# Kernel tuning notes

Hardware: AMD Instinct MI355X
Metric: run time of the kernel (lower is better)

Reference implementation:

```python
import jax, jax.numpy as jnp
import numpy as np
import math

B, S, D, H, DFF = 2, 2048, 1024, 16, 4096
DK = D // H
EPS = 1e-5


def setup_inputs() -> dict:
    key = jax.random.key(0)
    ks = jax.random.split(key, 8)
    s = 0.02
    return {
        "x": jax.random.normal(ks[0], (B, S, D), jnp.float32),
        "src_mask": jnp.ones((B, 1, 1, S), jnp.int32),
        "wq": jax.random.normal(ks[1], (D, D), jnp.float32) * s,
        "bq": jnp.zeros((D,), jnp.float32),
        "wk": jax.random.normal(ks[2], (D, D), jnp.float32) * s,
        "bk": jnp.zeros((D,), jnp.float32),
        "wv": jax.random.normal(ks[3], (D, D), jnp.float32) * s,
        "bv": jnp.zeros((D,), jnp.float32),
        "wo": jax.random.normal(ks[4], (D, D), jnp.float32) * s,
        "bo": jnp.zeros((D,), jnp.float32),
        "w1": jax.random.normal(ks[5], (DFF, D), jnp.float32) * s,
        "b1": jnp.zeros((DFF,), jnp.float32),
        "w2": jax.random.normal(ks[6], (D, DFF), jnp.float32) * s,
        "b2": jnp.zeros((D,), jnp.float32),
        "alpha1": jnp.ones((1,), jnp.float32),
        "bias1": jnp.ones((1,), jnp.float32),
        "alpha2": jnp.ones((1,), jnp.float32),
        "bias2": jnp.ones((1,), jnp.float32),
    }


def _layernorm(x, alpha, bias):
    # Faithful to source: unbiased std (ddof=1), divide by (std + eps),
    # scalar alpha/bias both initialized to 1.
    mean = jnp.mean(x, axis=-1, keepdims=True)
    std = jnp.std(x, axis=-1, keepdims=True, ddof=1)
    return alpha * (x - mean) / (std + EPS) + bias


def _mha(x, wq, bq, wk, bk, wv, bv, wo, bo):
    q = (x @ wq.T + bq).reshape(B, S, H, DK).swapaxes(1, 2)  # b h s d
    k = (x @ wk.T + bk).reshape(B, S, H, DK).swapaxes(1, 2)
    v = (x @ wv.T + bv).reshape(B, S, H, DK).swapaxes(1, 2)
    scores = jnp.einsum("bhqd,bhkd->bhqk", q, k) / math.sqrt(DK)
    # NOTE: source calls masked_fill (out-of-place) and discards the result,
    # so the mask has NO effect. Reproduced faithfully: no masking here.
    attn = jax.nn.softmax(scores, axis=-1)
    out = jnp.einsum("bhqk,bhkd->bhqd", attn, v)
    out = out.swapaxes(1, 2).reshape(B, S, D)
    return out @ wo.T + bo


def reference(x, src_mask, wq, bq, wk, bk, wv, bv, wo, bo,
              w1, b1, w2, b2, alpha1, bias1, alpha2, bias2):
    # residual[0]: x + attn(norm(x)) (dropout=0 -> identity)
    h1 = x + _mha(_layernorm(x, alpha1, bias1), wq, bq, wk, bk, wv, bv, wo, bo)
    # residual[1]: h1 + ffn(norm(h1))
    n2 = _layernorm(h1, alpha2, bias2)
    ffn = (n2 @ w1.T + b1) @ w2.T + b2
    return h1 + ffn
```

## Files before the change

kernel.cpp:

```cpp
#include <hip/hip_runtime.h>
#include <stdint.h>

#define Bx   2
#define Sx   2048
#define Dx   1024
#define Hx   16
#define DKx  64
#define DFFx 4096
#define Mx   4096

#define CEXP 0.18033688011112042f

typedef __attribute__((ext_vector_type(8))) short short8;
typedef __attribute__((ext_vector_type(4))) float f32x4;
typedef __attribute__((ext_vector_type(4))) unsigned short ushort4v;

__device__ __forceinline__ unsigned short f2b(float f) {
    union { float f; uint32_t u; } v; v.f = f;
    uint32_t u = v.u;
    u += 0x7fffu + ((u >> 16) & 1u);
    return (unsigned short)(u >> 16);
}

__device__ __forceinline__ float fexp2(float x) {
#if __has_builtin(__builtin_amdgcn_exp2f)
    return __builtin_amdgcn_exp2f(x);
#else
    return exp2f(x);
#endif
}

__global__ __launch_bounds__(256) void conv_all(
    const float4* __restrict__ wq, const float4* __restrict__ wk,
    const float4* __restrict__ wv, const float4* __restrict__ wo,
    const float4* __restrict__ w1, const float4* __restrict__ w2,
    const float4* __restrict__ bq, const float4* __restrict__ bk,
    const float4* __restrict__ bv,
    ushort4v* __restrict__ dqkv, ushort4v* __restrict__ dwo,
    ushort4v* __restrict__ d1, ushort4v* __restrict__ d2,
    float4* __restrict__ dbias) {
    const int i = blockIdx.x * 256 + threadIdx.x;
    const int S4 = 1 << 18;
    if (i < 4 * S4) {
        const float4* s; ushort4v* d;
        if (i < S4)          { s = wq + i;            d = dqkv + i; }
        else if (i < 2 * S4) { s = wk + (i - S4);     d = dqkv + i; }
        else if (i < 3 * S4) { s = wv + (i - 2 * S4); d = dqkv + i; }
        else                 { s = wo + (i - 3 * S4); d = dwo + (i - 3 * S4); }
        const float4 v = *s;
        ushort4v o; o.x = f2b(v.x); o.y = f2b(v.y); o.z = f2b(v.z); o.w = f2b(v.w);
        *d = o;
    } else if (i < 8 * S4) {
        const float4 v = w1[i - 4 * S4];
        ushort4v o; o.x = f2b(v.x); o.y = f2b(v.y); o.z = f2b(v.z); o.w = f2b(v.w);
        d1[i - 4 * S4] = o;
    } else if (i < 12 * S4) {
        const float4 v = w2[i - 8 * S4];
        ushort4v o; o.x = f2b(v.x); o.y = f2b(v.y); o.z = f2b(v.z); o.w = f2b(v.w);
        d2[i - 8 * S4] = o;
    } else if (i < 12 * S4 + 768) {
        const int jn = i - 12 * S4;
        dbias[jn] = (jn < 256) ? bq[jn] : (jn < 512 ? bk[jn - 256] : bv[jn - 512]);
    }
}

__global__ __launch_bounds__(256) void layernorm_k(const float* __restrict__ x,
                                                   const float* __restrict__ alpha,
                                                   const float* __restrict__ beta,
                                                   unsigned short* __restrict__ out) {
    __shared__ float red[8];
    const int row = blockIdx.x;
    const int t = threadIdx.x, lane = t & 63, w = t >> 6;
    float4 v = ((const float4*)(x + (size_t)row * Dx))[t];
    float s = v.x + v.y + v.z + v.w;
    float q = v.x*v.x + v.y*v.y + v.z*v.z + v.w*v.w;
#pragma unroll
    for (int off = 1; off < 64; off <<= 1) {
        s += __shfl_xor(s, off);
        q += __shfl_xor(q, off);
    }
    if (lane == 0) { red[w] = s; red[4 + w] = q; }
    __syncthreads();
    s = red[0] + red[1] + red[2] + red[3];
    q = red[4] + red[5] + red[6] + red[7];
    const float mean = s * (1.0f / Dx);
    float var = (q - (float)Dx * mean * mean) * (1.0f / (Dx - 1));
    var = fmaxf(var, 0.0f);
    const float inv = alpha[0] / (sqrtf(var) + 1e-5f);
    const float bb = beta[0];
    ushort4v o;
    o.x = f2b((v.x - mean) * inv + bb);
    o.y = f2b((v.y - mean) * inv + bb);
    o.z = f2b((v.z - mean) * inv + bb);
    o.w = f2b((v.w - mean) * inv + bb);
    *(ushort4v*)(out + (size_t)row * Dx + t * 4) = o;
}

#define GLDS(gp, lp) __builtin_amdgcn_global_load_lds( \
    (const __attribute__((address_space(1))) unsigned int*)(gp), \
    (__attribute__((address_space(3))) unsigned int*)(lp), 16, 0, 0)

#define STAGE(buf, kt) do {                                                     \
    const int k0_ = (kt) << 5;                                                  \
    _Pragma("unroll")                                                           \
    for (int i_ = 0; i_ < MB/2; ++i_) {                                         \
      const int ca_ = (MB==4) ? (w*2 + i_) : w;                                 \
      GLDS(A + (size_t)(bm + ca_*16 + srow)*K + k0_ + skc*8, &As[buf][ca_*512]);\
    }                                                                           \
    _Pragma("unroll")                                                           \
    for (int i_ = 0; i_ < 2; ++i_) {                                            \
      const int cb_ = w*2 + i_;                                                 \
      GLDS(W + (size_t)(bn + cb_*16 + srow)*K + k0_ + skc*8, &Bs[buf][cb_*512]);\
    }                                                                           \
  } while (0)

template<int BM>
__global__ __launch_bounds__(256) void gemm2(const short* __restrict__ A,
                                             const short* __restrict__ W,
                                             const float* __restrict__ bias,
                                             const float* __restrict__ res,
                                             float* __restrict__ Cout,
                                             int M, int N, int K) {
    constexpr int MB = BM / 32;
    __shared__ alignas(16) short As[2][BM * 32];
    __shared__ alignas(16) short Bs[2][128 * 32];
    const int t = threadIdx.x, lane = t & 63, w = t >> 6;
    const int bb = blockIdx.x, xcd = bb & 7, jj = bb >> 3;
    const int bn = (jj & 7) * 128;
    const int bm = (xcd * 8 + (jj >> 3)) * BM;
    const int wm = (w >> 1) * (BM / 2), wn = (w & 1) * 64;
    const int srow = lane >> 2, skc = lane & 3;

    f32x4 acc[MB][4] = {};
    const int nkt = K >> 5;

    STAGE(0, 0);
    __syncthreads();
    int cur = 0;
    for (int kt = 0; kt < nkt; ++kt) {
        if (kt + 1 < nkt) STAGE(cur ^ 1, kt + 1);
        const short* as = &As[cur][0];
        const short* bs = &Bs[cur][0];
        short8 af[MB], bfr[4];
#pragma unroll
        for (int mb = 0; mb < MB; ++mb)
            af[mb] = *(const short8*)&as[(wm + mb * 16 + (lane & 15)) * 32 + (lane >> 4) * 8];
#pragma unroll
        for (int nb = 0; nb < 4; ++nb)
            bfr[nb] = *(const short8*)&bs[(wn + nb * 16 + (lane & 15)) * 32 + (lane >> 4) * 8];
#pragma unroll
        for (int mb = 0; mb < MB; ++mb)
#pragma unroll
            for (int nb = 0; nb < 4; ++nb)
                acc[mb][nb] = __builtin_amdgcn_mfma_f32_16x16x32_bf16(af[mb], bfr[nb], acc[mb][nb], 0, 0, 0);
        __syncthreads();
        cur ^= 1;
    }

    const int r0 = (lane >> 4) * 4, c0 = lane & 15;
#pragma unroll
    for (int mb = 0; mb < MB; ++mb)
#pragma unroll
        for (int nb = 0; nb < 4; ++nb) {
            const int col = bn + wn + nb * 16 + c0;
            const float bv = bias[col];
            const int row0 = bm + wm + mb * 16 + r0;
#pragma unroll
            for (int r = 0; r < 4; ++r) {
                const size_t idx = (size_t)(row0 + r) * N + col;
                Cout[idx] = acc[mb][nb][r] + bv + res[idx];
            }
        }
}

template<int MODE>
__global__ __launch_bounds__(256) void gemm128(const short* __restrict__ A,
                                               const short* __restrict__ W,
                                               const float* __restrict__ bias,
                                               void* __restrict__ Cout,
                                               int N, int K,
                                               unsigned short* __restrict__ Qout,
                                               unsigned short* __restrict__ Kout,
                                               unsigned short* __restrict__ Vout) {
    constexpr int MB = 4;
    __shared__ alignas(16) short As[2][128 * 32];
    __shared__ alignas(16) short Bs[2][128 * 32];
    const int t = threadIdx.x, lane = t & 63, w = t >> 6;
    const int bb = blockIdx.x, bpx = gridDim.x >> 3;
    const int g = (bb & 7) * bpx + (bb >> 3);
    const int bn = (g >> 5) * 128;
    const int bm = (g & 31) * 128;
    const int wm = (w >> 1) * 64, wn = (w & 1) * 64;
    const int srow = lane >> 2, skc = lane & 3;

    f32x4 acc[MB][4] = {};
    const int nkt = K >> 5;

    STAGE(0, 0);
    __syncthreads();
    int cur = 0;
    for (int kt = 0; kt < nkt; ++kt) {
        if (kt + 1 < nkt) STAGE(cur ^ 1, kt + 1);
        const short* as = &As[cur][0];
        const short* bs = &Bs[cur][0];
        short8 af[MB], bfr[4];
#pragma unroll
        for (int mb = 0; mb < MB; ++mb)
            af[mb] = *(const short8*)&as[(wm + mb * 16 + (lane & 15)) * 32 + (lane >> 4) * 8];
#pragma unroll
        for (int nb = 0; nb < 4; ++nb)
            bfr[nb] = *(const short8*)&bs[(wn + nb * 16 + (lane & 15)) * 32 + (lane >> 4) * 8];
#pragma unroll
        for (int mb = 0; mb < MB; ++mb)
#pragma unroll
            for (int nb = 0; nb < 4; ++nb)
                acc[mb][nb] = __builtin_amdgcn_mfma_f32_16x16x32_bf16(af[mb], bfr[nb], acc[mb][nb], 0, 0, 0);
        __syncthreads();
        cur ^= 1;
    }

    const int r0 = (lane >> 4) * 4, c0 = lane & 15;
#pragma unroll
    for (int mb = 0; mb < MB; ++mb)
#pragma unroll
        for (int nb = 0; nb < 4; ++nb) {
            const int col = bn + wn + nb * 16 + c0;
            const float bv = bias[col];
            const int row0 = bm + wm + mb * 16 + r0;
            if (MODE == 0) {
#pragma unroll
                for (int r = 0; r < 4; ++r)
                    ((unsigned short*)Cout)[(size_t)(row0 + r) * N + col] = f2b(acc[mb][nb][r] + bv);
            } else {
                if (col < 1024) {
#pragma unroll
                    for (int r = 0; r < 4; ++r)
                        Qout[(size_t)(row0 + r) * 1024 + col] = f2b((acc[mb][nb][r] + bv) * CEXP);
                } else if (col < 2048) {
#pragma unroll
                    for (int r = 0; r < 4; ++r)
                        Kout[(size_t)(row0 + r) * 1024 + (col - 1024)] = f2b(acc[mb][nb][r] + bv);
                } else {
                    const int dk = col - 2048, hh = dk >> 6, dlo = dk & 63;
                    const int bbv = row0 >> 11, s0 = row0 & 2047;
                    const int vrow = (bbv * 16 + hh) * 64 + dlo;
                    ushort4v pv;
                    pv.x = f2b(acc[mb][nb][0] + bv);
                    pv.y = f2b(acc[mb][nb][1] + bv);
                    pv.z = f2b(acc[mb][nb][2] + bv);
                    pv.w = f2b(acc[mb][nb][3] + bv);
                    *(ushort4v*)&Vout[(size_t)vrow * Sx + s0] = pv;
                }
            }
        }
}

__global__ __launch_bounds__(256) void gemmsk(const short* __restrict__ A,
                                              const short* __restrict__ W,
                                              float* __restrict__ P0,
                                              float* __restrict__ P1,
                                              int K) {
    constexpr int MB = 4;
    __shared__ alignas(16) short As[2][128 * 32];
    __shared__ alignas(16) short Bs[2][128 * 32];
    const int t = threadIdx.x, lane = t & 63, w = t >> 6;
    const int bb = blockIdx.x, xcd = bb & 7, jj = bb >> 3;
    const int bn = (jj & 7) * 128;
    const int p = (xcd << 3) | (jj >> 3);
    const int bm = (p & 31) * 128;
    const int kz = p >> 5;
    float* __restrict__ P = kz ? P1 : P0;
    const int wm = (w >> 1) * 64, wn = (w & 1) * 64;
    const int srow = lane >> 2, skc = lane & 3;

    f32x4 acc[MB][4] = {};
    const int nkt = (K >> 1) >> 5;
    const int kbeg = kz * nkt;

    STAGE(0, kbeg);
    __syncthreads();
    int cur = 0;
    for (int kt = kbeg; kt < kbeg + nkt; ++kt) {
        if (kt + 1 < kbeg + nkt) STAGE(cur ^ 1, kt + 1);
        const short* as = &As[cur][0];
        const short* bs = &Bs[cur][0];
        short8 af[MB], bfr[4];
#pragma unroll
        for (int mb = 0; mb < MB; ++mb)
            af[mb] = *(const short8*)&as[(wm + mb * 16 + (lane & 15)) * 32 + (lane >> 4) * 8];
#pragma unroll
        for (int nb = 0; nb < 4; ++nb)
            bfr[nb] = *(const short8*)&bs[(wn + nb * 16 + (lane & 15)) * 32 + (lane >> 4) * 8];
#pragma unroll
        for (int mb = 0; mb < MB; ++mb)
#pragma unroll
            for (int nb = 0; nb < 4; ++nb)
                acc[mb][nb] = __builtin_amdgcn_mfma_f32_16x16x32_bf16(af[mb], bfr[nb], acc[mb][nb], 0, 0, 0);
        __syncthreads();
        cur ^= 1;
    }

    const int r0 = (lane >> 4) * 4, c0 = lane & 15;
#pragma unroll
    for (int mb = 0; mb < MB; ++mb)
#pragma unroll
        for (int nb = 0; nb < 4; ++nb) {
            const int col = bn + wn + nb * 16 + c0;
            const int row0 = bm + wm + mb * 16 + r0;
#pragma unroll
            for (int r = 0; r < 4; ++r)
                P[(size_t)(row0 + r) * Dx + col] = acc[mb][nb][r];
        }
}

__global__ __launch_bounds__(256) void epi2(const float4* __restrict__ p0,
                                            const float4* __restrict__ p1,
                                            const float4* __restrict__ b2,
                                            const float4* __restrict__ h1,
                                            float4* __restrict__ out) {
    const int i = blockIdx.x * 256 + threadIdx.x;
    const float4 bv = b2[i & 255];
    const float4 a = p0[i], b = p1[i], h = h1[i];
    float4 o;
    o.x = a.x + b.x + h.x + bv.x;
    o.y = a.y + b.y + h.y + bv.y;
    o.z = a.z + b.z + h.z + bv.z;
    o.w = a.w + b.w + h.w + bv.w;
    out[i] = o;
}

__global__ __launch_bounds__(256) void attn_fwd4(const short* __restrict__ Q,
                                                 const short* __restrict__ Kg,
                                                 const short* __restrict__ Vtg,
                                                 unsigned short* __restrict__ O) {
    __shared__ alignas(16) short Ks[64 * 64];
    __shared__ alignas(16) short Vs[64 * 64];
    __shared__ alignas(16) short Pl[4][32 * 64];
    const int t = threadIdx.x, lane = t & 63, w = t >> 6;
    const int bh = blockIdx.x;
    const int b = bh >> 4, h = bh & 15;
    const int q0 = blockIdx.y * 128 + w * 32;
    const int lo = lane & 15, hi = lane >> 4;

    short8 qf[2][2];
#pragma unroll
    for (int mb = 0; mb < 2; ++mb)
#pragma unroll
        for (int kf = 0; kf < 2; ++kf)
            qf[mb][kf] = *(const short8*)&Q[(size_t)(b * Sx + q0 + mb * 16 + lo) * Dx
                                            + h * DKx + kf * 32 + hi * 8];

    f32x4 o_[2][4] = {};
    f32x4 l_acc[2] = {};
    short8 ones;
#pragma unroll
    for (int j = 0; j < 8; ++j) ones[j] = (short)0x3F80;

    const int srow = t >> 2;
    const int scol2 = (t & 3) * 32;
    const int swz = (srow & 7) << 4;
    const short* Kbase = Kg + (size_t)(b * Sx) * Dx + h * DKx;
    const short* Vbase = Vtg + (size_t)(bh * 64 + srow) * Sx;
    char* KsB = (char*)Ks;
    char* VsB = (char*)Vs;
    char* PwB = (char*)&Pl[w][0];

    short8 kr0, kr1, vr0, vr1;
    {
        const short* kp = Kbase + (size_t)srow * Dx + (t & 3) * 16;
        kr0 = *(const short8*)kp; kr1 = *(const short8*)(kp + 8);
        const short* vp = Vbase + (t & 3) * 16;
        vr0 = *(const short8*)vp; vr1 = *(const short8*)(vp + 8);
    }

    for (int kt = 0; kt < Sx / 64; ++kt) {
        __syncthreads();
        *(short8*)(KsB + ((srow * 128 + scol2) ^ swz)) = kr0;
        *(short8*)(KsB + ((srow * 128 + scol2 + 16) ^ swz)) = kr1;
        *(short8*)(VsB + ((srow * 128 + scol2) ^ swz)) = vr0;
        *(short8*)(VsB + ((srow * 128 + scol2 + 16) ^ swz)) = vr1;
        __syncthreads();
        if (kt + 1 < Sx / 64) {
            const short* kp = Kbase + (size_t)((kt + 1) * 64 + srow) * Dx + (t & 3) * 16;
            kr0 = *(const short8*)kp; kr1 = *(const short8*)(kp + 8);
            const short* vp = Vbase + (kt + 1) * 64 + (t & 3) * 16;
            vr0 = *(const short8*)vp; vr1 = *(const short8*)(vp + 8);
        }

        f32x4 s[2][4] = {};
        __builtin_amdgcn_s_setprio(1);
#pragma unroll
        for (int nb = 0; nb < 4; ++nb) {
            const int key = nb * 16 + lo;
            const int ksw = (key & 7) << 4;
#pragma unroll
            for (int kf = 0; kf < 2; ++kf) {
                const short8 kfr = *(const short8*)(KsB + ((key * 128 + kf * 64 + hi * 16) ^ ksw));
#pragma unroll
                for (int mb = 0; mb < 2; ++mb)
                    s[mb][nb] = __builtin_amdgcn_mfma_f32_16x16x32_bf16(qf[mb][kf], kfr, s[mb][nb], 0, 0, 0);
            }
        }
        __builtin_amdgcn_s_setprio(0);

#pragma unroll
        for (int mb = 0; mb < 2; ++mb)
#pragma unroll
            for (int nb = 0; nb < 4; ++nb) {
                const int k = nb * 16 + lo;
#pragma unroll
                for (int r = 0; r < 4; ++r) {
                    const float p = fexp2(s[mb][nb][r]);
                    union { float f; uint32_t u; } cv; cv.f = p;
                    const int qq = mb * 16 + hi * 4 + r;
                    *(short*)(PwB + ((qq * 128 + k * 2) ^ ((qq & 7) << 4))) = (short)(cv.u >> 16);
                }
            }

        short8 pa[2][2];
#pragma unroll
        for (int mb = 0; mb < 2; ++mb)
#pragma unroll
            for (int kc = 0; kc < 2; ++kc)
                pa[mb][kc] = *(const short8*)(PwB + (((mb * 16 + lo) * 128 + kc * 64 + hi * 16) ^ ((lo & 7) << 4)));

        __builtin_amdgcn_s_setprio(1);
#pragma unroll
        for (int mb = 0; mb < 2; ++mb) {
            l_acc[mb] = __builtin_amdgcn_mfma_f32_16x16x32_bf16(pa[mb][0], ones, l_acc[mb], 0, 0, 0);
            l_acc[mb] = __builtin_amdgcn_mfma_f32_16x16x32_bf16(pa[mb][1], ones, l_acc[mb], 0, 0, 0);
        }

#pragma unroll
        for (int d = 0; d < 4; ++d) {
            const int vd = d * 16 + lo;
            const int vsw = (vd & 7) << 4;
#pragma unroll
            for (int kc = 0; kc < 2; ++kc) {
                const short8 vf = *(const short8*)(VsB + ((vd * 128 + kc * 64 + hi * 16) ^ vsw));
#pragma unroll
                for (int mb = 0; mb < 2; ++mb)
                    o_[mb][d] = __builtin_amdgcn_mfma_f32_16x16x32_bf16(pa[mb][kc], vf, o_[mb][d], 0, 0, 0);
            }
        }
        __builtin_amdgcn_s_setprio(0);
    }

#pragma unroll
    for (int mb = 0; mb < 2; ++mb)
#pragma unroll
        for (int d = 0; d < 4; ++d)
#pragma unroll
            for (int r = 0; r < 4; ++r) {
                const int qrow = b * Sx + q0 + mb * 16 + hi * 4 + r;
                O[(size_t)qrow * Dx + h * DKx + d * 16 + lo] = f2b(o_[mb][d][r] / l_acc[mb][r]);
            }
}

extern "C" void kernel_launch(void* const* d_in, const int* in_sizes, int n_in,
                              void* d_out, int out_size, void* d_ws, size_t ws_size,
                              hipStream_t stream) {
    const float* x  = (const float*)d_in[0];
    const float* wq = (const float*)d_in[2];
    const float* bq = (const float*)d_in[3];
    const float* wk = (const float*)d_in[4];
    const float* bk = (const float*)d_in[5];
    const float* wv = (const float*)d_in[6];
    const float* bv = (const float*)d_in[7];
    const float* wo = (const float*)d_in[8];
    const float* bo = (const float*)d_in[9];
    const float* w1 = (const float*)d_in[10];
    const float* b1 = (const float*)d_in[11];
    const float* w2 = (const float*)d_in[12];
    const float* b2 = (const float*)d_in[13];
    const float* alpha1 = (const float*)d_in[14];
    const float* bias1  = (const float*)d_in[15];
    const float* alpha2 = (const float*)d_in[16];
    const float* bias2  = (const float*)d_in[17];
    float* out = (float*)d_out;

    short* ws   = (short*)d_ws;
    short* wqkv = ws;
    short* wob  = wqkv + 3145728;
    short* w1b  = wob  + 1048576;
    short* w2b  = w1b  + 4194304;
    short* n1   = w2b  + 4194304;
    short* Qb   = n1   + 4194304;
    short* Kb   = Qb   + 4194304;
    short* Vt   = Kb   + 4194304;
    short* f1   = Vt   + 4194304;
    float* h1   = (float*)(f1 + 16777216);
    float* bqkv = (float*)((char*)h1 + ((size_t)Mx * Dx * 4));
    short* ao = n1;
    short* n2 = n1;
    float* p0 = (float*)n1;
    float* p1 = (float*)Kb;

    conv_all<<<12291, 256, 0, stream>>>((const float4*)wq, (const float4*)wk,
                                        (const float4*)wv, (const float4*)wo,
                                        (const float4*)w1, (const float4*)w2,
                                        (const float4*)bq, (const float4*)bk,
                                        (const float4*)bv,
                                        (ushort4v*)wqkv, (ushort4v*)wob,
                                        (ushort4v*)w1b, (ushort4v*)w2b,
                                        (float4*)bqkv);

    layernorm_k<<<Mx, 256, 0, stream>>>(x, alpha1, bias1, (unsigned short*)n1);

    gemm128<2><<<768, 256, 0, stream>>>(n1, wqkv, bqkv, nullptr, 3072, Dx,
                                        (unsigned short*)Qb, (unsigned short*)Kb,
                                        (unsigned short*)Vt);

    attn_fwd4<<<dim3(32, 16), 256, 0, stream>>>(Qb, Kb, Vt, (unsigned short*)ao);

    gemm2<64><<<512, 256, 0, stream>>>(ao, wob, bo, x, h1, Mx, Dx, Dx);

    layernorm_k<<<Mx, 256, 0, stream>>>(h1, alpha2, bias2, (unsigned short*)n2);

    gemm128<0><<<1024, 256, 0, stream>>>(n2, w1b, b1, f1, DFFx, Dx,
                                         nullptr, nullptr, nullptr);

    gemmsk<<<512, 256, 0, stream>>>(f1, w2b, p0, p1, DFFx);
    epi2<<<4096, 256, 0, stream>>>((const float4*)p0, (const float4*)p1,
                                   (const float4*)b2, (const float4*)h1, (float4*)out);
}
```

Before: 366.6 us.

## Load K and V fragments directly from global memory in attention, drop LDS staging

The attention kernel no longer stages K and V tiles through shared memory with block-wide barriers. Each wave now loads its MFMA operand fragments straight from global memory (K rows, transposed V). This removes the LDS writes, the LDS reads and both __syncthreads per key tile. In exchange, each of the four waves re-fetches the same K/V data from global memory or cache, the explicit register prefetch of the next tile is gone, and the V loads are strided rows that may be less coalesced.

```diff
diff --git a/kernel.cpp b/kernel.cpp
--- a/kernel.cpp
+++ b/kernel.cpp
@@ -329,12 +329,10 @@
     out[i] = o;
 }
 
-__global__ __launch_bounds__(256) void attn_fwd4(const short* __restrict__ Q,
+__global__ __launch_bounds__(256) void attn_fwd5(const short* __restrict__ Q,
                                                  const short* __restrict__ Kg,
                                                  const short* __restrict__ Vtg,
                                                  unsigned short* __restrict__ O) {
-    __shared__ alignas(16) short Ks[64 * 64];
-    __shared__ alignas(16) short Vs[64 * 64];
     __shared__ alignas(16) short Pl[4][32 * 64];
     const int t = threadIdx.x, lane = t & 63, w = t >> 6;
     const int bh = blockIdx.x;
@@ -356,52 +354,36 @@
 #pragma unroll
     for (int j = 0; j < 8; ++j) ones[j] = (short)0x3F80;
 
-    const int srow = t >> 2;
-    const int scol2 = (t & 3) * 32;
-    const int swz = (srow & 7) << 4;
-    const short* Kbase = Kg + (size_t)(b * Sx) * Dx + h * DKx;
-    const short* Vbase = Vtg + (size_t)(bh * 64 + srow) * Sx;
-    char* KsB = (char*)Ks;
-    char* VsB = (char*)Vs;
+    const short* Kb_ = Kg + (size_t)(b * Sx) * Dx + h * DKx;
+    const short* Vb_ = Vtg + (size_t)(bh * 64) * Sx;
     char* PwB = (char*)&Pl[w][0];
 
-    short8 kr0, kr1, vr0, vr1;
-    {
-        const short* kp = Kbase + (size_t)srow * Dx + (t & 3) * 16;
-        kr0 = *(const short8*)kp; kr1 = *(const short8*)(kp + 8);
-        const short* vp = Vbase + (t & 3) * 16;
-        vr0 = *(const short8*)vp; vr1 = *(const short8*)(vp + 8);
-    }
-
     for (int kt = 0; kt < Sx / 64; ++kt) {
-        __syncthreads();
-        *(short8*)(KsB + ((srow * 128 + scol2) ^ swz)) = kr0;
-        *(short8*)(KsB + ((srow * 128 + scol2 + 16) ^ swz)) = kr1;
-        *(short8*)(VsB + ((srow * 128 + scol2) ^ swz)) = vr0;
-        *(short8*)(VsB + ((srow * 128 + scol2 + 16) ^ swz)) = vr1;
-        __syncthreads();
-        if (kt + 1 < Sx / 64) {
-            const short* kp = Kbase + (size_t)((kt + 1) * 64 + srow) * Dx + (t & 3) * 16;
-            kr0 = *(const short8*)kp; kr1 = *(const short8*)(kp + 8);
-            const short* vp = Vbase + (kt + 1) * 64 + (t & 3) * 16;
-            vr0 = *(const short8*)vp; vr1 = *(const short8*)(vp + 8);
-        }
+        const short* Kt = Kb_ + (size_t)(kt * 64) * Dx;
+        short8 kfr[4][2];
+#pragma unroll
+        for (int nb = 0; nb < 4; ++nb)
+#pragma unroll
+            for (int kf = 0; kf < 2; ++kf)
+                kfr[nb][kf] = *(const short8*)&Kt[(size_t)(nb * 16 + lo) * Dx + kf * 32 + hi * 8];
 
         f32x4 s[2][4] = {};
         __builtin_amdgcn_s_setprio(1);
 #pragma unroll
-        for (int nb = 0; nb < 4; ++nb) {
-            const int key = nb * 16 + lo;
-            const int ksw = (key & 7) << 4;
-#pragma unroll
-            for (int kf = 0; kf < 2; ++kf) {
-                const short8 kfr = *(const short8*)(KsB + ((key * 128 + kf * 64 + hi * 16) ^ ksw));
+        for (int nb = 0; nb < 4; ++nb)
+#pragma unroll
+            for (int kf = 0; kf < 2; ++kf)
 #pragma unroll
                 for (int mb = 0; mb < 2; ++mb)
-                    s[mb][nb] = __builtin_amdgcn_mfma_f32_16x16x32_bf16(qf[mb][kf], kfr, s[mb][nb], 0, 0, 0);
-            }
-        }
+                    s[mb][nb] = __builtin_amdgcn_mfma_f32_16x16x32_bf16(qf[mb][kf], kfr[nb][kf], s[mb][nb], 0, 0, 0);
         __builtin_amdgcn_s_setprio(0);
+
+        short8 vf[4][2];
+#pragma unroll
+        for (int d = 0; d < 4; ++d)
+#pragma unroll
+            for (int kc = 0; kc < 2; ++kc)
+                vf[d][kc] = *(const short8*)&Vb_[(size_t)(d * 16 + lo) * Sx + kt * 64 + kc * 32 + hi * 8];
 
 #pragma unroll
         for (int mb = 0; mb < 2; ++mb)
@@ -432,17 +414,12 @@
         }
 
 #pragma unroll
-        for (int d = 0; d < 4; ++d) {
-            const int vd = d * 16 + lo;
-            const int vsw = (vd & 7) << 4;
-#pragma unroll
-            for (int kc = 0; kc < 2; ++kc) {
-                const short8 vf = *(const short8*)(VsB + ((vd * 128 + kc * 64 + hi * 16) ^ vsw));
+        for (int d = 0; d < 4; ++d)
+#pragma unroll
+            for (int kc = 0; kc < 2; ++kc)
 #pragma unroll
                 for (int mb = 0; mb < 2; ++mb)
-                    o_[mb][d] = __builtin_amdgcn_mfma_f32_16x16x32_bf16(pa[mb][kc], vf, o_[mb][d], 0, 0, 0);
-            }
-        }
+                    o_[mb][d] = __builtin_amdgcn_mfma_f32_16x16x32_bf16(pa[mb][kc], vf[d][kc], o_[mb][d], 0, 0, 0);
         __builtin_amdgcn_s_setprio(0);
     }
 
@@ -511,7 +488,7 @@
                                         (unsigned short*)Qb, (unsigned short*)Kb,
                                         (unsigned short*)Vt);
 
-    attn_fwd4<<<dim3(32, 16), 256, 0, stream>>>(Qb, Kb, Vt, (unsigned short*)ao);
+    attn_fwd5<<<dim3(32, 16), 256, 0, stream>>>(Qb, Kb, Vt, (unsigned short*)ao);
 
     gemm2<64><<<512, 256, 0, stream>>>(ao, wob, bo, x, h1, Mx, Dx, Dx);
 
```

Measured after the change: 423.9 us. +15.6%, slower.
